# Kernel optimization log

Measured on AMD Instinct MI355X. Metric: run time of the kernel, lower is better.

The kernel has to match this reference:

```python
import jax, jax.numpy as jnp
import numpy as np

B, F, V, E, A = 8192, 39, 1_000_000, 16, 16  # batch, fields, vocab, embed, attn


def setup_inputs() -> dict:
    key = jax.random.key(0)
    ks = jax.random.split(key, 9)
    return {
        "feat_index": jax.random.randint(ks[0], (B, F), 0, V),
        "feat_value": jax.random.uniform(ks[1], (B, F), dtype=jnp.float32),
        "first_order_weights": jax.random.normal(ks[2], (V, 1), dtype=jnp.float32) * 0.01,
        "emb_table": jax.random.normal(ks[3], (V, E), dtype=jnp.float32) * 0.01,
        "bias": jax.random.normal(ks[4], (1,), dtype=jnp.float32),
        "attention_w": jax.random.normal(ks[5], (E, A), dtype=jnp.float32) * 0.1,
        "attention_b": jax.random.normal(ks[6], (A,), dtype=jnp.float32) * 0.1,
        "projection_h": jax.random.normal(ks[7], (A, 1), dtype=jnp.float32) * 0.1,
        "projection_p": jax.random.normal(ks[8], (E, 1), dtype=jnp.float32) * 0.1,
    }


def reference(feat_index, feat_value, first_order_weights, emb_table, bias,
              attention_w, attention_b, projection_h, projection_p):
    fv = feat_value[..., None]                                  # [B,F,1]
    # first order: gather weights, scale by value, sum over fields
    y_first = jnp.sum(first_order_weights[feat_index] * fv, axis=1)[:, 0]  # [B]
    # embeddings scaled by feature values
    emb = emb_table[feat_index] * fv                            # [B,F,E]
    # pairwise bi-interaction over all i<j field pairs (num_pairs = F*(F-1)/2)
    iu, ju = np.triu_indices(F, k=1)
    bi = emb[:, iu, :] * emb[:, ju, :]                          # [B,P,E]
    # tiny attention MLP + softmax over pairs
    att = jax.nn.relu(jnp.einsum('bpe,ea->bpa', bi, attention_w) + attention_b)
    score = jax.nn.softmax(jnp.einsum('bpa,ao->bpo', att, projection_h), axis=1)  # [B,P,1]
    pooled = jnp.sum(score * bi, axis=1)                        # [B,E]
    aw = (pooled @ projection_p)[:, 0]                          # [B]
    y = bias + y_first + aw                                     # [B]
    return jax.nn.sigmoid(y)
```

## Files before the change

kernel.cpp:

```cpp
#include <hip/hip_runtime.h>
#include <math.h>


#define BB 8192
#define FF 39
#define PP 741
#define NT 24
#define RSTR 20
#define SSTR (FF * RSTR)

typedef short bf16x8 __attribute__((ext_vector_type(8)));
typedef float f32x4  __attribute__((ext_vector_type(4)));
typedef float f32x16 __attribute__((ext_vector_type(16)));

static __device__ __forceinline__ int pack2(float a, float b) {
    unsigned ua = __builtin_bit_cast(unsigned, a);
    unsigned ub = __builtin_bit_cast(unsigned, b);
    return (int)((ua >> 16) | (ub & 0xFFFF0000u));
}

__global__ __launch_bounds__(256)
void afm_kernel(const int*   __restrict__ fidx,
                const float* __restrict__ fval,
                const float* __restrict__ fow,
                const float* __restrict__ emb,
                const float* __restrict__ bias,
                const float* __restrict__ aw_,
                const float* __restrict__ ab_,
                const float* __restrict__ ph_,
                const float* __restrict__ pp_,
                float*       __restrict__ out)
{
    __shared__ __align__(16) float s_emb[4 * SSTR];
    __shared__ unsigned s_pij[NT * 32];

    const int tid  = threadIdx.x;
    const int wid  = tid >> 6;
    const int lane = tid & 63;
    const int n    = lane & 31;
    const int h    = lane >> 5;
    const int smp  = blockIdx.x * 4 + wid;

    if (tid < FF - 1) {
        int i = tid;
        int base = (i * (2 * FF - i - 1)) >> 1;
        for (int j = i + 1; j < FF; ++j)
            s_pij[base++] = ((unsigned)(i * 80) << 16) | (unsigned)(j * 80);
    } else if (tid == FF - 1) {
        for (int e = PP; e < NT * 32; ++e) s_pij[e] = 0u;
    }

    int ixr = 0; float vr = 0.f, fo = 0.f;
    if (lane < FF) {
        ixr = fidx[smp * FF + lane];
        vr  = fval[smp * FF + lane];
        fo  = fow[ixr] * vr;
    }
    #pragma unroll
    for (int m = 1; m < 64; m <<= 1) fo += __shfl_xor(fo, m);

    float* my = &s_emb[wid * SSTR];
    for (int u = lane; u < FF * 4; u += 64) {
        int row = u >> 2, q4 = u & 3;
        int   ix = __shfl(ixr, row);
        float v  = __shfl(vr,  row);
        const float4 ev = ((const float4*)emb)[(size_t)ix * 4 + q4];
        *(float4*)&my[row * RSTR + q4 * 4] =
            make_float4(ev.x * v, ev.y * v, ev.z * v, ev.w * v);
    }

    const f32x4 h_lo = ((const f32x4*)ph_)[h];
    const f32x4 h_hi = ((const f32x4*)ph_)[h + 2];

    f32x16 cinit;
    {
        const f32x4 ab_lo = ((const f32x4*)ab_)[h];
        const f32x4 ab_hi = ((const f32x4*)ab_)[h + 2];
        cinit[0] = ab_lo[0]; cinit[1] = ab_lo[1];
        cinit[2] = ab_lo[2]; cinit[3] = ab_lo[3];
        cinit[4] = ab_hi[0]; cinit[5] = ab_hi[1];
        cinit[6] = ab_hi[2]; cinit[7] = ab_hi[3];
        #pragma unroll
        for (int r = 8; r < 16; ++r) cinit[r] = 0.f;
    }

    bf16x8 wfrag;
    {
        float t0 = 0.f, t1 = 0.f, t2 = 0.f, t3 = 0.f,
              t4 = 0.f, t5 = 0.f, t6 = 0.f, t7 = 0.f;
        if (n < 16) {
            const float* base = aw_ + (8 * h) * 16 + n;
            t0 = base[0];   t1 = base[16];  t2 = base[32];  t3 = base[48];
            t4 = base[64];  t5 = base[80];  t6 = base[96];  t7 = base[112];
        }
        union { int i[4]; bf16x8 v; } u;
        u.i[0] = pack2(t0, t1); u.i[1] = pack2(t2, t3);
        u.i[2] = pack2(t4, t5); u.i[3] = pack2(t6, t7);
        wfrag = u.v;
    }

    __syncthreads();

    const char* bpre = (const char*)my + h * 32;
    float p0=0.f,p1=0.f,p2=0.f,p3=0.f,p4=0.f,p5=0.f,p6=0.f,p7=0.f;
    float z = 0.f;
    int pidx = n;
    #pragma unroll 4
    for (int t = 0; t < NT; ++t, pidx += 32) {
        unsigned pk = s_pij[t * 32 + n];
        const float4* ei = (const float4*)(bpre + (pk >> 16));
        const float4* ej = (const float4*)(bpre + (pk & 0xFFFFu));
        float4 a0 = ei[0], a1 = ei[1];
        float4 b0 = ej[0], b1 = ej[1];
        float m0 = a0.x*b0.x, m1 = a0.y*b0.y, m2 = a0.z*b0.z, m3 = a0.w*b0.w;
        float m4 = a1.x*b1.x, m5 = a1.y*b1.y, m6 = a1.z*b1.z, m7 = a1.w*b1.w;
        union { int i[4]; bf16x8 v; } u;
        u.i[0] = pack2(m0, m1); u.i[1] = pack2(m2, m3);
        u.i[2] = pack2(m4, m5); u.i[3] = pack2(m6, m7);
        f32x16 d = __builtin_amdgcn_mfma_f32_32x32x16_bf16(wfrag, u.v, cinit,
                                                           0, 0, 0);
        float s = fmaf(fmaxf(d[0], 0.f), h_lo[0],
                  fmaf(fmaxf(d[1], 0.f), h_lo[1],
                  fmaf(fmaxf(d[2], 0.f), h_lo[2],
                  fmaf(fmaxf(d[3], 0.f), h_lo[3],
                  fmaf(fmaxf(d[4], 0.f), h_hi[0],
                  fmaf(fmaxf(d[5], 0.f), h_hi[1],
                  fmaf(fmaxf(d[6], 0.f), h_hi[2],
                       fmaxf(d[7], 0.f) * h_hi[3])))))));
        s += __shfl_xor(s, 32);
        float w = __expf(s);
        w = (pidx < PP) ? w : 0.f;
        z += w;
        p0 = fmaf(w, m0, p0); p1 = fmaf(w, m1, p1);
        p2 = fmaf(w, m2, p2); p3 = fmaf(w, m3, p3);
        p4 = fmaf(w, m4, p4); p5 = fmaf(w, m5, p5);
        p6 = fmaf(w, m6, p6); p7 = fmaf(w, m7, p7);
    }

    const float4 pf0 = ((const float4*)pp_)[2 * h];
    const float4 pf1 = ((const float4*)pp_)[2 * h + 1];
    float awp = fmaf(p0, pf0.x, fmaf(p1, pf0.y, fmaf(p2, pf0.z,
                fmaf(p3, pf0.w, fmaf(p4, pf1.x, fmaf(p5, pf1.y,
                fmaf(p6, pf1.z, p7 * pf1.w)))))));
    #pragma unroll
    for (int m = 1; m < 64; m <<= 1) {
        awp += __shfl_xor(awp, m);
        z   += __shfl_xor(z, m);
    }
    if (lane == 0) {
        float y = bias[0] + fo + 2.f * awp / z;
        out[smp] = 1.f / (1.f + __expf(-y));
    }
}

extern "C" void kernel_launch(void* const* d_in, const int* in_sizes, int n_in,
                              void* d_out, int out_size, void* d_ws, size_t ws_size,
                              hipStream_t stream) {
    const int*   fidx      = (const int*)  d_in[0];
    const float* fval      = (const float*)d_in[1];
    const float* fow       = (const float*)d_in[2];
    const float* emb_table = (const float*)d_in[3];
    const float* bias      = (const float*)d_in[4];
    const float* attn_w    = (const float*)d_in[5];
    const float* attn_b    = (const float*)d_in[6];
    const float* proj_h    = (const float*)d_in[7];
    const float* proj_p    = (const float*)d_in[8];
    float* out = (float*)d_out;

    afm_kernel<<<BB / 4, 256, 0, stream>>>(fidx, fval, fow, emb_table, bias,
                                           attn_w, attn_b, proj_h, proj_p, out);
}
```

Measured before the change: 132.6 us.

## Store scaled embeddings as bf16 in LDS and streamline pair loop

Embeddings are scaled by feature values, packed to bf16, and stored in LDS with a 48-byte row stride, so each pair needs a single 16-byte load per operand instead of two float4 loads. Packing uses v_perm, the exponent uses exp2 with log2e folded into the projection weights, and the tail mask is applied only to the last tile. The intent is to cut LDS traffic and ALU work in the inner loop. Elementwise products are now formed from bf16-rounded inputs, which adds rounding error to the pooled result.

Result: no change. 132.7 us (+0.1%).

```diff
diff --git a/kernel.cpp b/kernel.cpp
--- a/kernel.cpp
+++ b/kernel.cpp
@@ -6,17 +6,23 @@
 #define FF 39
 #define PP 741
 #define NT 24
-#define RSTR 20
-#define SSTR (FF * RSTR)
+#define RBYTES 48
+#define SBYTES (FF * RBYTES)
 
 typedef short bf16x8 __attribute__((ext_vector_type(8)));
 typedef float f32x4  __attribute__((ext_vector_type(4)));
 typedef float f32x16 __attribute__((ext_vector_type(16)));
 
-static __device__ __forceinline__ int pack2(float a, float b) {
-    unsigned ua = __builtin_bit_cast(unsigned, a);
-    unsigned ub = __builtin_bit_cast(unsigned, b);
-    return (int)((ua >> 16) | (ub & 0xFFFF0000u));
+static __device__ __forceinline__ unsigned pack2(float lo, float hi) {
+    return __builtin_amdgcn_perm(__builtin_bit_cast(unsigned, hi),
+                                 __builtin_bit_cast(unsigned, lo),
+                                 0x07060302u);
+}
+static __device__ __forceinline__ float up_lo(unsigned d) {
+    return __builtin_bit_cast(float, d << 16);
+}
+static __device__ __forceinline__ float up_hi(unsigned d) {
+    return __builtin_bit_cast(float, d & 0xFFFF0000u);
 }
 
 __global__ __launch_bounds__(256)
@@ -31,7 +37,7 @@
                 const float* __restrict__ pp_,
                 float*       __restrict__ out)
 {
-    __shared__ __align__(16) float s_emb[4 * SSTR];
+    __shared__ __align__(16) unsigned char s_emb[4 * SBYTES];
     __shared__ unsigned s_pij[NT * 32];
 
     const int tid  = threadIdx.x;
@@ -45,7 +51,7 @@
         int i = tid;
         int base = (i * (2 * FF - i - 1)) >> 1;
         for (int j = i + 1; j < FF; ++j)
-            s_pij[base++] = ((unsigned)(i * 80) << 16) | (unsigned)(j * 80);
+            s_pij[base++] = ((unsigned)(i * RBYTES) << 16) | (unsigned)(j * RBYTES);
     } else if (tid == FF - 1) {
         for (int e = PP; e < NT * 32; ++e) s_pij[e] = 0u;
     }
@@ -59,18 +65,25 @@
     #pragma unroll
     for (int m = 1; m < 64; m <<= 1) fo += __shfl_xor(fo, m);
 
-    float* my = &s_emb[wid * SSTR];
-    for (int u = lane; u < FF * 4; u += 64) {
-        int row = u >> 2, q4 = u & 3;
+    unsigned char* my = s_emb + wid * SBYTES;
+    for (int u = lane; u < FF * 2; u += 64) {
+        int row = u >> 1, hh = u & 1;
         int   ix = __shfl(ixr, row);
         float v  = __shfl(vr,  row);
-        const float4 ev = ((const float4*)emb)[(size_t)ix * 4 + q4];
-        *(float4*)&my[row * RSTR + q4 * 4] =
-            make_float4(ev.x * v, ev.y * v, ev.z * v, ev.w * v);
+        const float4* src = (const float4*)emb + (size_t)ix * 4 + hh * 2;
+        float4 e0 = src[0], e1 = src[1];
+        uint4 d = make_uint4(pack2(e0.x * v, e0.y * v),
+                             pack2(e0.z * v, e0.w * v),
+                             pack2(e1.x * v, e1.y * v),
+                             pack2(e1.z * v, e1.w * v));
+        *(uint4*)(my + row * RBYTES + hh * 16) = d;
     }
 
-    const f32x4 h_lo = ((const f32x4*)ph_)[h];
-    const f32x4 h_hi = ((const f32x4*)ph_)[h + 2];
+    const float LOG2E = 1.44269504088896f;
+    f32x4 h_lo = ((const f32x4*)ph_)[h];
+    f32x4 h_hi = ((const f32x4*)ph_)[h + 2];
+    #pragma unroll
+    for (int r = 0; r < 4; ++r) { h_lo[r] *= LOG2E; h_hi[r] *= LOG2E; }
 
     f32x16 cinit;
     {
@@ -93,7 +106,7 @@
             t0 = base[0];   t1 = base[16];  t2 = base[32];  t3 = base[48];
             t4 = base[64];  t5 = base[80];  t6 = base[96];  t7 = base[112];
         }
-        union { int i[4]; bf16x8 v; } u;
+        union { unsigned i[4]; bf16x8 v; } u;
         u.i[0] = pack2(t0, t1); u.i[1] = pack2(t2, t3);
         u.i[2] = pack2(t4, t5); u.i[3] = pack2(t6, t7);
         wfrag = u.v;
@@ -101,41 +114,52 @@
 
     __syncthreads();
 
-    const char* bpre = (const char*)my + h * 32;
+    const unsigned char* bpre = my + h * 16;
+    const unsigned* pijp = s_pij + n;
     float p0=0.f,p1=0.f,p2=0.f,p3=0.f,p4=0.f,p5=0.f,p6=0.f,p7=0.f;
     float z = 0.f;
-    int pidx = n;
+
+#define TILE(PK, MASKED, MOK)                                             \
+    {                                                                     \
+        unsigned pk = (PK);                                               \
+        uint4 di = *(const uint4*)(bpre + (pk >> 16));                    \
+        uint4 dj = *(const uint4*)(bpre + (pk & 0xFFFFu));                \
+        float m0 = up_lo(di.x) * up_lo(dj.x);                             \
+        float m1 = up_hi(di.x) * up_hi(dj.x);                             \
+        float m2 = up_lo(di.y) * up_lo(dj.y);                             \
+        float m3 = up_hi(di.y) * up_hi(dj.y);                             \
+        float m4 = up_lo(di.z) * up_lo(dj.z);                             \
+        float m5 = up_hi(di.z) * up_hi(dj.z);                             \
+        float m6 = up_lo(di.w) * up_lo(dj.w);                             \
+        float m7 = up_hi(di.w) * up_hi(dj.w);                             \
+        union { unsigned i[4]; bf16x8 v; } u;                             \
+        u.i[0] = pack2(m0, m1); u.i[1] = pack2(m2, m3);                   \
+        u.i[2] = pack2(m4, m5); u.i[3] = pack2(m6, m7);                   \
+        f32x16 d = __builtin_amdgcn_mfma_f32_32x32x16_bf16(wfrag, u.v,    \
+                                                           cinit, 0, 0, 0); \
+        float s = fmaf(fmaxf(d[0], 0.f), h_lo[0],                         \
+                  fmaf(fmaxf(d[1], 0.f), h_lo[1],                         \
+                  fmaf(fmaxf(d[2], 0.f), h_lo[2],                         \
+                  fmaf(fmaxf(d[3], 0.f), h_lo[3],                         \
+                  fmaf(fmaxf(d[4], 0.f), h_hi[0],                         \
+                  fmaf(fmaxf(d[5], 0.f), h_hi[1],                         \
+                  fmaf(fmaxf(d[6], 0.f), h_hi[2],                         \
+                       fmaxf(d[7], 0.f) * h_hi[3])))))));                 \
+        s += __shfl_xor(s, 32);                                           \
+        float w = __builtin_amdgcn_exp2f(s);                              \
+        if (MASKED) w = (MOK) ? w : 0.f;                                  \
+        z += w;                                                           \
+        p0 = fmaf(w, m0, p0); p1 = fmaf(w, m1, p1);                       \
+        p2 = fmaf(w, m2, p2); p3 = fmaf(w, m3, p3);                       \
+        p4 = fmaf(w, m4, p4); p5 = fmaf(w, m5, p5);                       \
+        p6 = fmaf(w, m6, p6); p7 = fmaf(w, m7, p7);                       \
+    }
+
     #pragma unroll 4
-    for (int t = 0; t < NT; ++t, pidx += 32) {
-        unsigned pk = s_pij[t * 32 + n];
-        const float4* ei = (const float4*)(bpre + (pk >> 16));
-        const float4* ej = (const float4*)(bpre + (pk & 0xFFFFu));
-        float4 a0 = ei[0], a1 = ei[1];
-        float4 b0 = ej[0], b1 = ej[1];
-        float m0 = a0.x*b0.x, m1 = a0.y*b0.y, m2 = a0.z*b0.z, m3 = a0.w*b0.w;
-        float m4 = a1.x*b1.x, m5 = a1.y*b1.y, m6 = a1.z*b1.z, m7 = a1.w*b1.w;
-        union { int i[4]; bf16x8 v; } u;
-        u.i[0] = pack2(m0, m1); u.i[1] = pack2(m2, m3);
-        u.i[2] = pack2(m4, m5); u.i[3] = pack2(m6, m7);
-        f32x16 d = __builtin_amdgcn_mfma_f32_32x32x16_bf16(wfrag, u.v, cinit,
-                                                           0, 0, 0);
-        float s = fmaf(fmaxf(d[0], 0.f), h_lo[0],
-                  fmaf(fmaxf(d[1], 0.f), h_lo[1],
-                  fmaf(fmaxf(d[2], 0.f), h_lo[2],
-                  fmaf(fmaxf(d[3], 0.f), h_lo[3],
-                  fmaf(fmaxf(d[4], 0.f), h_hi[0],
-                  fmaf(fmaxf(d[5], 0.f), h_hi[1],
-                  fmaf(fmaxf(d[6], 0.f), h_hi[2],
-                       fmaxf(d[7], 0.f) * h_hi[3])))))));
-        s += __shfl_xor(s, 32);
-        float w = __expf(s);
-        w = (pidx < PP) ? w : 0.f;
-        z += w;
-        p0 = fmaf(w, m0, p0); p1 = fmaf(w, m1, p1);
-        p2 = fmaf(w, m2, p2); p3 = fmaf(w, m3, p3);
-        p4 = fmaf(w, m4, p4); p5 = fmaf(w, m5, p5);
-        p6 = fmaf(w, m6, p6); p7 = fmaf(w, m7, p7);
-    }
+    for (int t = 0; t < NT - 1; ++t)
+        TILE(pijp[t * 32], false, true);
+    TILE(pijp[(NT - 1) * 32], true, (n < PP - (NT - 1) * 32));
+#undef TILE
 
     const float4 pf0 = ((const float4*)pp_)[2 * h];
     const float4 pf1 = ((const float4*)pp_)[2 * h + 1];
```
